# Optimization experiments

Measured on AMD Instinct MI355X. Metric: run time of the kernel, lower is better.

Reference implementation:

```python
import jax, jax.numpy as jnp
import numpy as np
from jax import lax


def conv3d(x, w, b):
    # x: (B,W,D,H,Cin), w: (kW,kD,kH,Cin,Cout), 'same' padding, stride 1
    return lax.conv_general_dilated(
        x, w, window_strides=(1, 1, 1), padding='SAME',
        dimension_numbers=('NDHWC', 'DHWIO', 'NDHWC')) + b


def proj(x, w, b, s, o):
    # Conv3D -> BatchNorm (inference, folded to per-channel affine) -> ReLU
    return jax.nn.relu(conv3d(x, w, b) * s + o)


def setup_inputs() -> dict:
    key = jax.random.key(0)
    ks = jax.random.split(key, 6)
    B, W, D, H, C = 2, 16, 16, 16, 32
    WS = 0.05  # weight scale to keep sigmoid of the NxN chain unsaturated
    return {
        'x': jax.random.normal(ks[0], (B, W, D, H, C), jnp.float32),
        'gamma': jax.random.uniform(ks[1], (1,), jnp.float32),
        'q_w': jax.random.normal(ks[2], (1, 3, 1, C, 8), jnp.float32) * WS,
        'q_b': jnp.zeros((8,), jnp.float32),
        'q_s': jnp.ones((8,), jnp.float32),
        'q_o': jnp.zeros((8,), jnp.float32),
        'k_w': jax.random.normal(ks[3], (3, 1, 1, C, 8), jnp.float32) * WS,
        'k_b': jnp.zeros((8,), jnp.float32),
        'k_s': jnp.ones((8,), jnp.float32),
        'k_o': jnp.zeros((8,), jnp.float32),
        'j_w': jax.random.normal(ks[4], (1, 1, 3, C, 8), jnp.float32) * WS,
        'j_b': jnp.zeros((8,), jnp.float32),
        'j_s': jnp.ones((8,), jnp.float32),
        'j_o': jnp.zeros((8,), jnp.float32),
        'v_w': jax.random.normal(ks[5], (1, 1, 1, C, C), jnp.float32) * WS,
        'v_b': jnp.zeros((C,), jnp.float32),
        'v_s': jnp.ones((C,), jnp.float32),
        'v_o': jnp.zeros((C,), jnp.float32),
    }


def reference(x, gamma, q_w, q_b, q_s, q_o, k_w, k_b, k_s, k_o,
              j_w, j_b, j_s, j_o, v_w, v_b, v_s, v_o):
    B, W, D, H, C = x.shape
    N = W * D * H
    # Q/K/J: (B,W,D,H,8) -> row-major reshape to (B,8,N) exactly as tf Reshape
    Qt = jnp.swapaxes(proj(x, q_w, q_b, q_s, q_o).reshape(B, -1, N), 1, 2)  # (B,N,8)
    K = proj(x, k_w, k_b, k_s, k_o).reshape(B, -1, N)                        # (B,8,N)
    Jt = jnp.swapaxes(proj(x, j_w, j_b, j_s, j_o).reshape(B, -1, N), 1, 2)  # (B,N,8)
    V = proj(x, v_w, v_b, v_s, v_o).reshape(B, N, -1)                        # (B,N,C)
    m1 = jnp.matmul(Qt, K)          # (B,N,N)
    m2 = jnp.matmul(Jt, K)          # (B,N,N)
    affinity = jax.nn.sigmoid(jnp.matmul(m1, m2))  # (B,N,N)
    weights = jnp.matmul(affinity, V).reshape(B, W, D, H, C)
    return gamma * weights + x
```

## Files before the change

### kernel.cpp

```cpp
#include <hip/hip_runtime.h>
#include <cstddef>

#define NN 4096

typedef short bf16x8 __attribute__((ext_vector_type(8)));
typedef float f32x4 __attribute__((ext_vector_type(4)));

__device__ __forceinline__ unsigned pack_bf16(float a, float b) {
    const unsigned ua = __float_as_uint(a) + 0x8000u;
    const unsigned ub = __float_as_uint(b) + 0x8000u;
    return (ua >> 16) | (ub & 0xffff0000u);
}
__device__ __forceinline__ unsigned short f2bf(float f) {
    return (unsigned short)((__float_as_uint(f) + 0x8000u) >> 16);
}

__global__ __launch_bounds__(256) void kA(
    const float* __restrict__ x,
    const float* __restrict__ qw, const float* __restrict__ qb,
    const float* __restrict__ qs, const float* __restrict__ qo,
    const float* __restrict__ kw, const float* __restrict__ kb,
    const float* __restrict__ ks, const float* __restrict__ ko,
    const float* __restrict__ jw, const float* __restrict__ jb,
    const float* __restrict__ js, const float* __restrict__ jo,
    const float* __restrict__ vw, const float* __restrict__ vb,
    const float* __restrict__ vs, const float* __restrict__ vo,
    float* __restrict__ Qf, float* __restrict__ Kf,
    unsigned short* __restrict__ Vt, float* __restrict__ Mm)
{
    __shared__ float vw_s[1024];
    __shared__ float cw_s[3 * 776];
    __shared__ float Kl[16][8];
    __shared__ float Jl[16][8];
    const int t = threadIdx.x;

    ((float4*)vw_s)[t] = ((const float4*)vw)[t];
    if (t < 192) {
        ((float4*)(cw_s))[t]              = ((const float4*)qw)[t];
        ((float4*)(cw_s + 776))[t]        = ((const float4*)kw)[t];
        ((float4*)(cw_s + 1552))[t]       = ((const float4*)jw)[t];
    }
    __syncthreads();

    const int spi = t >> 4;
    const int g   = t & 15;
    const int gsp = blockIdx.x * 16 + spi;
    const int b   = gsp >> 12;
    const int sp  = gsp & 4095;
    const int w = sp >> 8, d = (sp >> 4) & 15, h = sp & 15;

    if (g < 8) {
        const int c4 = g;
        const float4* xr = (const float4*)(x + (size_t)gsp * 32);
        float4 acc = make_float4(0.f, 0.f, 0.f, 0.f);
        #pragma unroll
        for (int c8 = 0; c8 < 8; ++c8) {
            const float4 xv = xr[c8];
            #pragma unroll
            for (int k = 0; k < 4; ++k) {
                const float xs = (k == 0) ? xv.x : (k == 1) ? xv.y : (k == 2) ? xv.z : xv.w;
                const float4 wv = *(const float4*)&vw_s[(c8 * 4 + k) * 32 + c4 * 4];
                acc.x += xs * wv.x; acc.y += xs * wv.y;
                acc.z += xs * wv.z; acc.w += xs * wv.w;
            }
        }
        const float4 bb = ((const float4*)vb)[c4];
        const float4 sc = ((const float4*)vs)[c4];
        const float4 oo = ((const float4*)vo)[c4];
        float4 r;
        r.x = fmaxf((acc.x + bb.x) * sc.x + oo.x, 0.f);
        r.y = fmaxf((acc.y + bb.y) * sc.y + oo.y, 0.f);
        r.z = fmaxf((acc.z + bb.z) * sc.z + oo.z, 0.f);
        r.w = fmaxf((acc.w + bb.w) * sc.w + oo.w, 0.f);
        unsigned short* vt = Vt + (size_t)b * 131072 + (size_t)(c4 * 4) * 4096 + sp;
        vt[0]        = f2bf(r.x);
        vt[4096]     = f2bf(r.y);
        vt[2 * 4096] = f2bf(r.z);
        vt[3 * 4096] = f2bf(r.w);
    } else if (g < 14) {
        const int gg   = g - 8;
        const int conv = gg >> 1;
        const int co4  = gg & 1;
        const int coord  = (conv == 0) ? d : (conv == 1) ? w : h;
        const int stride = (conv == 0) ? 16 : (conv == 1) ? 256 : 1;
        const float* cw = cw_s + conv * 776;
        float4 acc = make_float4(0.f, 0.f, 0.f, 0.f);
        #pragma unroll
        for (int tap = 0; tap < 3; ++tap) {
            const int cc = coord + tap - 1;
            if (cc < 0 || cc > 15) continue;
            const float4* xt = (const float4*)(x + (size_t)(gsp + (tap - 1) * stride) * 32);
            #pragma unroll
            for (int c8 = 0; c8 < 8; ++c8) {
                const float4 xv = xt[c8];
                #pragma unroll
                for (int k = 0; k < 4; ++k) {
                    const float xs = (k == 0) ? xv.x : (k == 1) ? xv.y : (k == 2) ? xv.z : xv.w;
                    const float4 wv = *(const float4*)&cw[tap * 256 + (c8 * 4 + k) * 8 + co4 * 4];
                    acc.x += xs * wv.x; acc.y += xs * wv.y;
                    acc.z += xs * wv.z; acc.w += xs * wv.w;
                }
            }
        }
        const float* bbp = (conv == 0) ? qb : (conv == 1) ? kb : jb;
        const float* scp = (conv == 0) ? qs : (conv == 1) ? ks : js;
        const float* oop = (conv == 0) ? qo : (conv == 1) ? ko : jo;
        const float4 bb = ((const float4*)bbp)[co4];
        const float4 sc = ((const float4*)scp)[co4];
        const float4 oo = ((const float4*)oop)[co4];
        float4 r;
        r.x = fmaxf((acc.x + bb.x) * sc.x + oo.x, 0.f);
        r.y = fmaxf((acc.y + bb.y) * sc.y + oo.y, 0.f);
        r.z = fmaxf((acc.z + bb.z) * sc.z + oo.z, 0.f);
        r.w = fmaxf((acc.w + bb.w) * sc.w + oo.w, 0.f);
        if (conv == 0) {
            ((float4*)(Qf + (size_t)b * 32768 + (size_t)sp * 8))[co4] = r;
        } else if (conv == 1) {
            ((float4*)(Kf + (size_t)b * 32768 + (size_t)sp * 8))[co4] = r;
            *(float4*)&Kl[spi][co4 * 4] = r;
        } else {
            *(float4*)&Jl[spi][co4 * 4] = r;
        }
    }

    __syncthreads();
    if (t < 64) {
        const int r = t >> 3, s = t & 7;
        float acc = 0.f;
        #pragma unroll
        for (int i = 0; i < 16; ++i) acc += Kl[i][r] * Jl[i][s];
        atomicAdd(&Mm[b * 64 + t], acc);
    }
}

__global__ __launch_bounds__(256) void kD(
    const float* __restrict__ Qf, const float* __restrict__ Mm,
    const float* __restrict__ Kf, const unsigned short* __restrict__ Vt,
    const float* __restrict__ xin,
    const float* __restrict__ gamma, float* __restrict__ out)
{
    const int blk = blockIdx.x;
    const int jsp = blk & 7;
    const int rt  = (blk >> 3) & 63;
    const int b   = blk >> 9;
    const int i0  = rt * 64;
    const int j0  = jsp * 512;
    const int t   = threadIdx.x;
    const int jg = t & 15, rg = t >> 4;
    const int w = t >> 6, lane = t & 63;
    const int m = lane & 15, quad = lane >> 4;

    __shared__ float m_s[64];
    __shared__ unsigned short s_lds[2][64][72];

    if (t < 64) m_s[t] = Mm[b * 64 + t];
    __syncthreads();

    float P[4][8];
    {
        float a[4][8];
        #pragma unroll
        for (int r = 0; r < 8; ++r) {
            const float* qr = Qf + (size_t)b * 32768 + (size_t)r * 4096 + i0 + rg * 4;
            #pragma unroll
            for (int ri = 0; ri < 4; ++ri) a[ri][r] = qr[ri];
        }
        #pragma unroll
        for (int s = 0; s < 8; ++s) {
            #pragma unroll
            for (int ri = 0; ri < 4; ++ri) {
                float acc = 0.f;
                #pragma unroll
                for (int r = 0; r < 8; ++r) acc += a[ri][r] * m_s[r * 8 + s];
                P[ri][s] = acc;
            }
        }
    }

    const float* Kb = Kf + (size_t)b * 32768;
    const unsigned short* Vb = Vt + (size_t)b * 131072;

    f32x4 acc0 = {0.f, 0.f, 0.f, 0.f};
    f32x4 acc1 = {0.f, 0.f, 0.f, 0.f};

    for (int jc = 0; jc < 8; ++jc) {
        const int jb = j0 + jc * 64;
        float4 kr[8];
        #pragma unroll
        for (int r = 0; r < 8; ++r)
            kr[r] = *(const float4*)(Kb + (size_t)r * 4096 + jb + jg * 4);
        const float* krf = (const float*)kr;

        float sv[4][4];
        #pragma unroll
        for (int jt = 0; jt < 4; ++jt) {
            #pragma unroll
            for (int ri = 0; ri < 4; ++ri) {
                float dsum = 0.f;
                #pragma unroll
                for (int r = 0; r < 8; ++r) dsum += P[ri][r] * krf[r * 4 + jt];
                sv[ri][jt] = __builtin_amdgcn_rcpf(1.0f + __expf(-dsum));
            }
        }
        #pragma unroll
        for (int ri = 0; ri < 4; ++ri) {
            *(uint2*)&s_lds[jc & 1][rg * 4 + ri][jg * 4] =
                make_uint2(pack_bf16(sv[ri][0], sv[ri][1]),
                           pack_bf16(sv[ri][2], sv[ri][3]));
        }
        __syncthreads();
        #pragma unroll
        for (int kt = 0; kt < 2; ++kt) {
            const bf16x8 af = *(const bf16x8*)&s_lds[jc & 1][w * 16 + m][kt * 32 + quad * 8];
            {
                const bf16x8 bv = *(const bf16x8*)(Vb + (size_t)m * 4096 + jb + kt * 32 + quad * 8);
                acc0 = __builtin_amdgcn_mfma_f32_16x16x32_bf16(af, bv, acc0, 0, 0, 0);
            }
            {
                const bf16x8 bv = *(const bf16x8*)(Vb + (size_t)(16 + m) * 4096 + jb + kt * 32 + quad * 8);
                acc1 = __builtin_amdgcn_mfma_f32_16x16x32_bf16(af, bv, acc1, 0, 0, 0);
            }
        }
    }

    const float g = gamma[0];
    #pragma unroll
    for (int reg = 0; reg < 4; ++reg) {
        const int row = i0 + w * 16 + quad * 4 + reg;
        float* op = out + ((size_t)b * 4096 + row) * 32 + m;
        float add0 = g * acc0[reg];
        float add1 = g * acc1[reg];
        if (jsp == 0) {
            add0 += xin[((size_t)b * 4096 + row) * 32 + m];
            add1 += xin[((size_t)b * 4096 + row) * 32 + m + 16];
        }
        atomicAdd(op,      add0);
        atomicAdd(op + 16, add1);
    }
}

extern "C" void kernel_launch(void* const* d_in, const int* in_sizes, int n_in,
                              void* d_out, int out_size, void* d_ws, size_t ws_size,
                              hipStream_t stream)
{
    const float* x     = (const float*)d_in[0];
    const float* gamma = (const float*)d_in[1];
    const float* qw = (const float*)d_in[2];
    const float* qb = (const float*)d_in[3];
    const float* qs = (const float*)d_in[4];
    const float* qo = (const float*)d_in[5];
    const float* kw = (const float*)d_in[6];
    const float* kb = (const float*)d_in[7];
    const float* ks = (const float*)d_in[8];
    const float* ko = (const float*)d_in[9];
    const float* jw = (const float*)d_in[10];
    const float* jb = (const float*)d_in[11];
    const float* js = (const float*)d_in[12];
    const float* jo = (const float*)d_in[13];
    const float* vw = (const float*)d_in[14];
    const float* vb = (const float*)d_in[15];
    const float* vs = (const float*)d_in[16];
    const float* vo = (const float*)d_in[17];

    float* ws = (float*)d_ws;
    float* Qf = ws;
    float* Kf = ws + 65536;
    float* Mm = ws + 131072;
    unsigned short* Vt = (unsigned short*)(ws + 131200);

    kA<<<512, 256, 0, stream>>>(x, qw, qb, qs, qo, kw, kb, ks, ko,
                                jw, jb, js, jo, vw, vb, vs, vo,
                                Qf, Kf, Vt, Mm);
    kD<<<1024, 256, 0, stream>>>(Qf, Mm, Kf, Vt, x, gamma, (float*)d_out);
}
```

Baseline: 129.3 us.

## Replace atomic split-K output accumulation with partial buffer and reduction kernel

The attention kernel no longer atomically adds its split-K partial results into the output. Each block writes its 64x32 partial tile to a workspace buffer, and a new kernel sums the 8 partials and applies gamma and the residual add. This removes global float atomics and the reliance on the output starting at zero, at the cost of an extra launch and about 2 MB of extra traffic. It also vectorises the Q loads to float4 and unrolls the j-chunk loop by 2.

```diff
diff --git a/kernel.cpp b/kernel.cpp
--- a/kernel.cpp
+++ b/kernel.cpp
@@ -36,9 +36,9 @@
 
     ((float4*)vw_s)[t] = ((const float4*)vw)[t];
     if (t < 192) {
-        ((float4*)(cw_s))[t]              = ((const float4*)qw)[t];
-        ((float4*)(cw_s + 776))[t]        = ((const float4*)kw)[t];
-        ((float4*)(cw_s + 1552))[t]       = ((const float4*)jw)[t];
+        ((float4*)(cw_s))[t]        = ((const float4*)qw)[t];
+        ((float4*)(cw_s + 776))[t]  = ((const float4*)kw)[t];
+        ((float4*)(cw_s + 1552))[t] = ((const float4*)jw)[t];
     }
     __syncthreads();
 
@@ -136,8 +136,7 @@
 __global__ __launch_bounds__(256) void kD(
     const float* __restrict__ Qf, const float* __restrict__ Mm,
     const float* __restrict__ Kf, const unsigned short* __restrict__ Vt,
-    const float* __restrict__ xin,
-    const float* __restrict__ gamma, float* __restrict__ out)
+    float* __restrict__ Pt)
 {
     const int blk = blockIdx.x;
     const int jsp = blk & 7;
@@ -161,9 +160,8 @@
         float a[4][8];
         #pragma unroll
         for (int r = 0; r < 8; ++r) {
-            const float* qr = Qf + (size_t)b * 32768 + (size_t)r * 4096 + i0 + rg * 4;
-            #pragma unroll
-            for (int ri = 0; ri < 4; ++ri) a[ri][r] = qr[ri];
+            const float4 qv = *(const float4*)(Qf + (size_t)b * 32768 + (size_t)r * 4096 + i0 + rg * 4);
+            a[0][r] = qv.x; a[1][r] = qv.y; a[2][r] = qv.z; a[3][r] = qv.w;
         }
         #pragma unroll
         for (int s = 0; s < 8; ++s) {
@@ -183,6 +181,7 @@
     f32x4 acc0 = {0.f, 0.f, 0.f, 0.f};
     f32x4 acc1 = {0.f, 0.f, 0.f, 0.f};
 
+    #pragma unroll 2
     for (int jc = 0; jc < 8; ++jc) {
         const int jb = j0 + jc * 64;
         float4 kr[8];
@@ -223,20 +222,37 @@
         }
     }
 
-    const float g = gamma[0];
+    float* pp = Pt + (((size_t)(b * 64 + rt)) * 8 + jsp) * 2048;
     #pragma unroll
     for (int reg = 0; reg < 4; ++reg) {
-        const int row = i0 + w * 16 + quad * 4 + reg;
-        float* op = out + ((size_t)b * 4096 + row) * 32 + m;
-        float add0 = g * acc0[reg];
-        float add1 = g * acc1[reg];
-        if (jsp == 0) {
-            add0 += xin[((size_t)b * 4096 + row) * 32 + m];
-            add1 += xin[((size_t)b * 4096 + row) * 32 + m + 16];
-        }
-        atomicAdd(op,      add0);
-        atomicAdd(op + 16, add1);
-    }
+        const int rowin = w * 16 + quad * 4 + reg;
+        pp[rowin * 32 + m]      = acc0[reg];
+        pp[rowin * 32 + m + 16] = acc1[reg];
+    }
+}
+
+__global__ __launch_bounds__(256) void kE(
+    const float* __restrict__ Pt, const float* __restrict__ xin,
+    const float* __restrict__ gamma, float* __restrict__ out)
+{
+    const int f    = blockIdx.x * 256 + threadIdx.x;
+    const int tile = f >> 9;
+    const int fin  = f & 511;
+    const float4* base = (const float4*)(Pt + (size_t)tile * 8 * 2048) + fin;
+    float4 s = base[0];
+    #pragma unroll
+    for (int j = 1; j < 8; ++j) {
+        const float4 v = base[(size_t)j * 512];
+        s.x += v.x; s.y += v.y; s.z += v.z; s.w += v.w;
+    }
+    const float g = gamma[0];
+    const float4 xv = ((const float4*)xin)[f];
+    float4 r;
+    r.x = g * s.x + xv.x;
+    r.y = g * s.y + xv.y;
+    r.z = g * s.z + xv.z;
+    r.w = g * s.w + xv.w;
+    ((float4*)out)[f] = r;
 }
 
 extern "C" void kernel_launch(void* const* d_in, const int* in_sizes, int n_in,
@@ -267,9 +283,11 @@
     float* Kf = ws + 65536;
     float* Mm = ws + 131072;
     unsigned short* Vt = (unsigned short*)(ws + 131200);
+    float* Pt = ws + 262272;
 
     kA<<<512, 256, 0, stream>>>(x, qw, qb, qs, qo, kw, kb, ks, ko,
                                 jw, jb, js, jo, vw, vb, vs, vo,
                                 Qf, Kf, Vt, Mm);
-    kD<<<1024, 256, 0, stream>>>(Qf, Mm, Kf, Vt, x, gamma, (float*)d_out);
-}
+    kD<<<1024, 256, 0, stream>>>(Qf, Mm, Kf, Vt, Pt);
+    kE<<<256, 256, 0, stream>>>(Pt, x, gamma, (float*)d_out);
+}
```

After: 133.9 us. 3.5% more time.

## Split conv taps across threads and double grid parallelism in both kernels

Applied to the files above, without the earlier changes.

The projection kernel now gives each spatial point 32 threads, so each conv tap runs on its own thread. Tap partial sums are reduced through shared memory before the affine and ReLU step, which lifts the block count from 512 to 1024. The attention kernel splits the key range into 16 chunks instead of 8, doubling the grid to 2048 blocks, unrolls the now-shorter chunk loop, and loads Q as float4. This trades more blocks, an extra barrier and more partial-output traffic in the second kernel for better occupancy and latency hiding.

```diff
diff --git a/kernel.cpp b/kernel.cpp
--- a/kernel.cpp
+++ b/kernel.cpp
@@ -30,21 +30,22 @@
 {
     __shared__ float vw_s[1024];
     __shared__ float cw_s[3 * 776];
-    __shared__ float Kl[16][8];
-    __shared__ float Jl[16][8];
+    __shared__ float4 tap_s[8][18];
+    __shared__ float Kl[8][8];
+    __shared__ float Jl[8][8];
     const int t = threadIdx.x;
 
     ((float4*)vw_s)[t] = ((const float4*)vw)[t];
     if (t < 192) {
-        ((float4*)(cw_s))[t]              = ((const float4*)qw)[t];
-        ((float4*)(cw_s + 776))[t]        = ((const float4*)kw)[t];
-        ((float4*)(cw_s + 1552))[t]       = ((const float4*)jw)[t];
-    }
-    __syncthreads();
-
-    const int spi = t >> 4;
-    const int g   = t & 15;
-    const int gsp = blockIdx.x * 16 + spi;
+        ((float4*)(cw_s))[t]        = ((const float4*)qw)[t];
+        ((float4*)(cw_s + 776))[t]  = ((const float4*)kw)[t];
+        ((float4*)(cw_s + 1552))[t] = ((const float4*)jw)[t];
+    }
+    __syncthreads();
+
+    const int spi = t >> 5;
+    const int g   = t & 31;
+    const int gsp = blockIdx.x * 8 + spi;
     const int b   = gsp >> 12;
     const int sp  = gsp & 4095;
     const int w = sp >> 8, d = (sp >> 4) & 15, h = sp & 15;
@@ -77,31 +78,44 @@
         vt[4096]     = f2bf(r.y);
         vt[2 * 4096] = f2bf(r.z);
         vt[3 * 4096] = f2bf(r.w);
-    } else if (g < 14) {
-        const int gg   = g - 8;
-        const int conv = gg >> 1;
-        const int co4  = gg & 1;
+    } else if (g < 26) {
+        const int u    = g - 8;
+        const int conv = u / 6;
+        const int rem  = u % 6;
+        const int co4  = rem / 3;
+        const int tap  = rem % 3;
         const int coord  = (conv == 0) ? d : (conv == 1) ? w : h;
         const int stride = (conv == 0) ? 16 : (conv == 1) ? 256 : 1;
-        const float* cw = cw_s + conv * 776;
         float4 acc = make_float4(0.f, 0.f, 0.f, 0.f);
-        #pragma unroll
-        for (int tap = 0; tap < 3; ++tap) {
-            const int cc = coord + tap - 1;
-            if (cc < 0 || cc > 15) continue;
+        const int cc = coord + tap - 1;
+        if (cc >= 0 && cc <= 15) {
             const float4* xt = (const float4*)(x + (size_t)(gsp + (tap - 1) * stride) * 32);
+            const float* cw = cw_s + conv * 776 + tap * 256 + co4 * 4;
             #pragma unroll
             for (int c8 = 0; c8 < 8; ++c8) {
                 const float4 xv = xt[c8];
                 #pragma unroll
                 for (int k = 0; k < 4; ++k) {
                     const float xs = (k == 0) ? xv.x : (k == 1) ? xv.y : (k == 2) ? xv.z : xv.w;
-                    const float4 wv = *(const float4*)&cw[tap * 256 + (c8 * 4 + k) * 8 + co4 * 4];
+                    const float4 wv = *(const float4*)&cw[(c8 * 4 + k) * 8];
                     acc.x += xs * wv.x; acc.y += xs * wv.y;
                     acc.z += xs * wv.z; acc.w += xs * wv.w;
                 }
             }
         }
+        tap_s[spi][u] = acc;
+    }
+    __syncthreads();
+
+    if (g >= 26) {
+        const int cu   = g - 26;
+        const int conv = cu >> 1;
+        const int co4  = cu & 1;
+        const float4 a0 = tap_s[spi][conv * 6 + co4 * 3 + 0];
+        const float4 a1 = tap_s[spi][conv * 6 + co4 * 3 + 1];
+        const float4 a2 = tap_s[spi][conv * 6 + co4 * 3 + 2];
+        float4 acc = make_float4(a0.x + a1.x + a2.x, a0.y + a1.y + a2.y,
+                                 a0.z + a1.z + a2.z, a0.w + a1.w + a2.w);
         const float* bbp = (conv == 0) ? qb : (conv == 1) ? kb : jb;
         const float* scp = (conv == 0) ? qs : (conv == 1) ? ks : js;
         const float* oop = (conv == 0) ? qo : (conv == 1) ? ko : jo;
@@ -128,7 +142,7 @@
         const int r = t >> 3, s = t & 7;
         float acc = 0.f;
         #pragma unroll
-        for (int i = 0; i < 16; ++i) acc += Kl[i][r] * Jl[i][s];
+        for (int i = 0; i < 8; ++i) acc += Kl[i][r] * Jl[i][s];
         atomicAdd(&Mm[b * 64 + t], acc);
     }
 }
@@ -140,11 +154,11 @@
     const float* __restrict__ gamma, float* __restrict__ out)
 {
     const int blk = blockIdx.x;
-    const int jsp = blk & 7;
-    const int rt  = (blk >> 3) & 63;
-    const int b   = blk >> 9;
+    const int jsp = blk & 15;
+    const int rt  = (blk >> 4) & 63;
+    const int b   = blk >> 10;
     const int i0  = rt * 64;
-    const int j0  = jsp * 512;
+    const int j0  = jsp * 256;
     const int t   = threadIdx.x;
     const int jg = t & 15, rg = t >> 4;
     const int w = t >> 6, lane = t & 63;
@@ -161,9 +175,8 @@
         float a[4][8];
         #pragma unroll
         for (int r = 0; r < 8; ++r) {
-            const float* qr = Qf + (size_t)b * 32768 + (size_t)r * 4096 + i0 + rg * 4;
-            #pragma unroll
-            for (int ri = 0; ri < 4; ++ri) a[ri][r] = qr[ri];
+            const float4 qv = *(const float4*)(Qf + (size_t)b * 32768 + (size_t)r * 4096 + i0 + rg * 4);
+            a[0][r] = qv.x; a[1][r] = qv.y; a[2][r] = qv.z; a[3][r] = qv.w;
         }
         #pragma unroll
         for (int s = 0; s < 8; ++s) {
@@ -183,7 +196,8 @@
     f32x4 acc0 = {0.f, 0.f, 0.f, 0.f};
     f32x4 acc1 = {0.f, 0.f, 0.f, 0.f};
 
-    for (int jc = 0; jc < 8; ++jc) {
+    #pragma unroll
+    for (int jc = 0; jc < 4; ++jc) {
         const int jb = j0 + jc * 64;
         float4 kr[8];
         #pragma unroll
@@ -268,8 +282,8 @@
     float* Mm = ws + 131072;
     unsigned short* Vt = (unsigned short*)(ws + 131200);
 
-    kA<<<512, 256, 0, stream>>>(x, qw, qb, qs, qo, kw, kb, ks, ko,
-                                jw, jb, js, jo, vw, vb, vs, vo,
-                                Qf, Kf, Vt, Mm);
-    kD<<<1024, 256, 0, stream>>>(Qf, Mm, Kf, Vt, x, gamma, (float*)d_out);
-}
+    kA<<<1024, 256, 0, stream>>>(x, qw, qb, qs, qo, kw, kb, ks, ko,
+                                 jw, jb, js, jo, vw, vb, vs, vo,
+                                 Qf, Kf, Vt, Mm);
+    kD<<<2048, 256, 0, stream>>>(Qf, Mm, Kf, Vt, x, gamma, (float*)d_out);
+}
```

Result: slower. 146.7 us (+13.4%).
